# Optimization experiments

Hardware: AMD Instinct MI355X
Metric: run time of the kernel (lower is better)

Reference implementation:

```python
import jax, jax.numpy as jnp
import numpy as np

B, S, C, DM, NH, DH = 1, 2048, 2048, 768, 12, 64
LN_EPS = 1e-9


def setup_inputs() -> dict:
    rng = jax.random.key(0)
    ks = jax.random.split(rng, 24)
    f32 = jnp.float32
    p = 0.02  # param init scale
    inp = {
        'query': jax.random.normal(ks[0], (B, S, DM), f32),
        'key': jax.random.normal(ks[1], (B, C, DM), f32),
        'value': jax.random.normal(ks[2], (B, C, DM), f32),
        'phi': jax.random.normal(ks[3], (S, DM), f32) * p,
        'pi': jax.random.normal(ks[4], (S, DM), f32) * p,
        'psi': jax.random.normal(ks[5], (C, DM), f32) * p,
        'omega': jax.random.normal(ks[6], (C, DM), f32) * p,
        'cls_mask': jnp.ones((S, C), f32),
        'token_type_mat': jax.random.randint(ks[7], (B, S, C), 0, 2).astype(bool),
        'attention_mask': jnp.ones((B, C), jnp.int32),
        # learned parameters
        'Wq': jax.random.normal(ks[8], (DM, NH * DH), f32) * p,
        'Wk': jax.random.normal(ks[9], (DM, NH * DH), f32) * p,
        'bk': jnp.zeros((NH * DH,), f32),
        'Wv': jax.random.normal(ks[10], (DM, NH * DH), f32) * p,
        'bv': jnp.zeros((NH * DH,), f32),
        'r_w_bias': jax.random.normal(ks[11], (NH, DH), f32) * p,
        'r_r_bias': jax.random.normal(ks[12], (NH, DH), f32) * p,
        'r_kernel': jax.random.normal(ks[13], (DM, NH, DH), f32) * p,
        'r_s_bias': jax.random.normal(ks[14], (NH, DH), f32) * p,
        'seg_embed': jax.random.normal(ks[15], (2, NH, DH), f32) * p,
        'Wo': jax.random.normal(ks[16], (NH * DH, DM), f32) * p,
        'bo': jnp.zeros((DM,), f32),
        'ln_scale': jnp.ones((DM,), f32),
        'ln_bias': jnp.zeros((DM,), f32),
    }
    return inp


def reference(query, key, value, phi, pi, psi, omega, cls_mask,
              token_type_mat, attention_mask,
              Wq, Wk, bk, Wv, bv, r_w_bias, r_r_bias, r_kernel,
              r_s_bias, seg_embed, Wo, bo, ln_scale, ln_bias):
    b, s, _ = query.shape
    c = key.shape[1]
    scale = 1.0 / DH ** 0.5
    # head projections
    q = (query @ Wq).reshape(b, s, NH, DH) * scale          # [b,i,n,h]
    k = (key @ Wk + bk).reshape(b, c, NH, DH)                # [b,j,n,h]
    v = (value @ Wv + bv).reshape(b, c, NH, DH)
    # content score
    content = jnp.einsum('binh,bjnh->bnij', q + r_w_bias * scale, k)
    # factorized relative positional attention
    qr = jnp.einsum('binh,dnh->bind', q + r_r_bias * scale, r_kernel)  # [b,i,n,d_model]
    pos = (jnp.einsum('bind,jd->bnij', qr * phi[:, None], psi)
           + jnp.einsum('bind,jd->bnij', qr * pi[:, None], omega))
    pos = pos * cls_mask
    # token-type attention
    tt_bias = jnp.einsum('binh,snh->bnis', q + r_s_bias * scale, seg_embed)  # [b,n,i,2]
    diff_tt, same_tt = jnp.split(tt_bias, 2, axis=-1)  # each [b,n,i,1]
    tt = jnp.where(token_type_mat[:, None], same_tt, diff_tt) * cls_mask
    # combine, mask, softmax
    score = content + pos + tt
    score = score - 1000000.0 * (1.0 - attention_mask[:, None, None].astype(jnp.float32))
    prob = jax.nn.softmax(score, axis=-1)  # [b,n,i,j]
    attn_vec = jnp.einsum('bnij,bjnh->binh', prob, v).reshape(b, s, NH * DH)
    attn_out = attn_vec @ Wo + bo
    # residual + layernorm
    x = query + attn_out
    mu = x.mean(-1, keepdims=True)
    var = x.var(-1, keepdims=True)
    return (x - mu) * jax.lax.rsqrt(var + LN_EPS) * ln_scale + ln_bias
```

## Files before the change

kernel.cpp:

```cpp
#include <hip/hip_runtime.h>
#include <hip/hip_bf16.h>
#include <stddef.h>

#define DEVINL __device__ __forceinline__

typedef __attribute__((ext_vector_type(8))) short short8;
typedef __attribute__((ext_vector_type(4))) float f32x4;

static constexpr int S_LEN = 2048;
static constexpr int C_LEN = 2048;
static constexpr int DMODEL = 768;
static constexpr int NHEAD = 12;
static constexpr int DHEAD = 64;
static constexpr float SCALE = 0.125f;

DEVINL float bf2f(short s) {
    union { unsigned u; float f; } v;
    v.u = ((unsigned)(unsigned short)s) << 16;
    return v.f;
}
DEVINL short f2bf(float f) {
    union { float f; unsigned u; } v;
    v.f = f;
    unsigned r = v.u + 0x7FFFu + ((v.u >> 16) & 1u);
    return (short)(r >> 16);
}
DEVINL f32x4 zero4() { f32x4 z; z[0]=0.f; z[1]=0.f; z[2]=0.f; z[3]=0.f; return z; }

DEVINL int swz(int width, int row, int col) {
    return (row * width + col) ^ ((row & 7) << 3);
}

DEVINL void gl_lds16(const short* g, short* l) {
    __builtin_amdgcn_global_load_lds(
        (const __attribute__((address_space(1))) void*)g,
        (__attribute__((address_space(3))) void*)l,
        16, 0, 0);
}

template<int ROWS, int WIDTH>
DEVINL void stage_lds_swz(short* lds_tile, const short* src, int src_stride, int w, int lane) {
    constexpr int CPR = WIDTH / 8;
    constexpr int CH  = ROWS * CPR;
    for (int c0 = w * 64; c0 < CH; c0 += 256) {
        int chunk = c0 + lane;
        int row   = chunk / CPR;
        int ccol  = chunk % CPR;
        int scol  = ccol ^ (row & 7);
        gl_lds16(src + (size_t)row * src_stride + scol * 8, lds_tile + c0 * 8);
    }
}

DEVINL void stage_addcol(short* dst, const short* src, const float* p1, const float* p2,
                         int col0, int src_stride) {
    for (int c = threadIdx.x; c < 1024; c += 256) {
        int row = c >> 3;
        int cc  = (c & 7) * 8;
        short8 a = *(const short8*)(src + (size_t)row * src_stride + cc);
        short8 r;
#pragma unroll
        for (int e = 0; e < 8; ++e)
            r[e] = f2bf(bf2f(a[e]) + (p1[col0 + cc + e] - p2[col0 + cc + e]) * SCALE);
        *(short8*)(dst + swz(64, row, cc)) = r;
    }
}

DEVINL void mfma_step_128(const short* As, const short* Bs, f32x4 acc[4][4],
                          int wr, int wc, int lane) {
#pragma unroll
    for (int kk = 0; kk < 64; kk += 32) {
        short8 a[4], b[4];
#pragma unroll
        for (int mi = 0; mi < 4; ++mi)
            a[mi] = *(const short8*)(As + swz(64, wr*64 + mi*16 + (lane & 15), kk + (lane >> 4) * 8));
#pragma unroll
        for (int ni = 0; ni < 4; ++ni)
            b[ni] = *(const short8*)(Bs + swz(64, wc*64 + ni*16 + (lane & 15), kk + (lane >> 4) * 8));
#pragma unroll
        for (int mi = 0; mi < 4; ++mi)
#pragma unroll
            for (int ni = 0; ni < 4; ++ni)
                acc[mi][ni] = __builtin_amdgcn_mfma_f32_16x16x32_bf16(a[mi], b[ni], acc[mi][ni], 0, 0, 0);
    }
}

DEVINL void mfma_row16(const short* As, const short* Bs, f32x4 acc[8], int w, int lane) {
#pragma unroll
    for (int kk = 0; kk < 64; kk += 32) {
        short8 a = *(const short8*)(As + swz(64, w*16 + (lane & 15), kk + (lane >> 4) * 8));
#pragma unroll
        for (int nj = 0; nj < 8; ++nj) {
            short8 b = *(const short8*)(Bs + swz(64, nj*16 + (lane & 15), kk + (lane >> 4) * 8));
            acc[nj] = __builtin_amdgcn_mfma_f32_16x16x32_bf16(a, b, acc[nj], 0, 0, 0);
        }
    }
}

template<int KSTEPS>
DEVINL void gemm128_body(const short* A, const short* Bt, short* As, short* Bs,
                         f32x4 acc[4][4], int wr, int wc, int lane, int w) {
    for (int ks = 0; ks < KSTEPS; ++ks) {
        if (ks) __syncthreads();
        stage_lds_swz<128, 64>(As, A + ks * 64, DMODEL, w, lane);
        stage_lds_swz<128, 64>(Bs, Bt + ks * 64, DMODEL, w, lane);
        __syncthreads();
        mfma_step_128(As, Bs, acc, wr, wc, lane);
    }
}

__global__ void conv_kernel(const float* q, const float* k, const float* v,
                            const float* psi, const float* omega, const float* rk,
                            short* qc, short* kc, short* vc,
                            short* psc, short* omc, short* rkc) {
    int z = blockIdx.z;
    const float* src; short* dst; int n4;
    switch (z) {
        case 0: src = q;     dst = qc;  n4 = 393216; break;
        case 1: src = k;     dst = kc;  n4 = 393216; break;
        case 2: src = v;     dst = vc;  n4 = 393216; break;
        case 3: src = psi;   dst = psc; n4 = 393216; break;
        case 4: src = omega; dst = omc; n4 = 393216; break;
        default: src = rk;   dst = rkc; n4 = 147456; break;
    }
    for (int i = blockIdx.x * 256 + threadIdx.x; i < n4; i += gridDim.x * 256) {
        float4 f = *(const float4*)(src + (size_t)i * 4);
        short4 o;
        o.x = f2bf(f.x); o.y = f2bf(f.y); o.z = f2bf(f.z); o.w = f2bf(f.w);
        *(short4*)(dst + (size_t)i * 4) = o;
    }
}

__global__ void transpose_kernel(const float* wq, const float* wk, const float* wv, const float* wo,
                                 short* wqt, short* wkt, short* wvt, short* wot) {
    __shared__ float tile[64][65];
    int z = blockIdx.z;
    const float* src = (z == 0) ? wq : (z == 1) ? wk : (z == 2) ? wv : wo;
    short*       dst = (z == 0) ? wqt : (z == 1) ? wkt : (z == 2) ? wvt : wot;
    int r0 = blockIdx.x * 64, c0 = blockIdx.y * 64;
    for (int e = threadIdx.x; e < 4096; e += 256) {
        int rr = e >> 6, cc = e & 63;
        tile[rr][cc] = src[(size_t)(r0 + rr) * DMODEL + c0 + cc];
    }
    __syncthreads();
    for (int e = threadIdx.x; e < 4096; e += 256) {
        int rr = e >> 6, cc = e & 63;
        dst[(size_t)(c0 + rr) * DMODEL + r0 + cc] = f2bf(tile[cc][rr]);
    }
}

__global__ __launch_bounds__(256, 2)
void qkv_kernel(const short* qc, const short* kc, const short* vc,
                const short* wqt, const short* wkt, const short* wvt,
                const float* bk, const float* bv, const float* rw,
                short* qw_a, short* kpack, short* vt) {
    __shared__ short As[128 * 64], Bs[128 * 64];
    int z = blockIdx.z;
    const short* A  = (z == 0) ? qc  : (z == 1) ? kc  : vc;
    const short* Bt = (z == 0) ? wqt : (z == 1) ? wkt : wvt;
    int i0 = blockIdx.x * 128, c0 = blockIdx.y * 128;
    int t = threadIdx.x, lane = t & 63, w = t >> 6, wr = w >> 1, wc = w & 1;

    f32x4 acc[4][4];
#pragma unroll
    for (int mi = 0; mi < 4; ++mi)
#pragma unroll
        for (int ni = 0; ni < 4; ++ni) acc[mi][ni] = zero4();

    gemm128_body<12>(A + (size_t)i0 * DMODEL, Bt + (size_t)c0 * DMODEL, As, Bs, acc, wr, wc, lane, w);

#pragma unroll
    for (int mi = 0; mi < 4; ++mi)
#pragma unroll
        for (int ni = 0; ni < 4; ++ni)
#pragma unroll
            for (int r = 0; r < 4; ++r) {
                int row = i0 + wr*64 + mi*16 + ((lane >> 4) << 2) + r;
                int col = c0 + wc*64 + ni*16 + (lane & 15);
                float v = acc[mi][ni][r];
                if (z == 0) {
                    qw_a[(size_t)row * DMODEL + col] = f2bf(v * SCALE + rw[col] * SCALE);
                } else if (z == 1) {
                    float vv = v + bk[col];
                    kpack[((size_t)(col >> 6) * C_LEN + row) * DHEAD + (col & 63)] = f2bf(vv);
                } else {
                    float vv = v + bv[col];
                    vt[((size_t)(col >> 6) * DHEAD + (col & 63)) * C_LEN + row] = f2bf(vv);
                }
            }
}

__global__ __launch_bounds__(256, 2)
void qr_kernel(const short* qwa, const short* rkc, const float* rr, const float* rw,
               const float* phi, const float* pi_, short* a1, short* a2, int n_base) {
    __shared__ short As[128 * 64], Bs[128 * 64];
    int nl = blockIdx.z, n = n_base + nl;
    int i0 = blockIdx.x * 128, d0 = blockIdx.y * 128;
    int t = threadIdx.x, lane = t & 63, w = t >> 6, wr = w >> 1, wc = w & 1;

    f32x4 acc[4][4];
#pragma unroll
    for (int mi = 0; mi < 4; ++mi)
#pragma unroll
        for (int ni = 0; ni < 4; ++ni) acc[mi][ni] = zero4();

    stage_addcol(As, qwa + (size_t)i0 * DMODEL + n * DHEAD, rr, rw, n * DHEAD, DMODEL);
    stage_lds_swz<128, 64>(Bs, rkc + (size_t)d0 * DMODEL + n * DHEAD, DMODEL, w, lane);
    __syncthreads();
    mfma_step_128(As, Bs, acc, wr, wc, lane);

#pragma unroll
    for (int mi = 0; mi < 4; ++mi)
#pragma unroll
        for (int ni = 0; ni < 4; ++ni)
#pragma unroll
            for (int r = 0; r < 4; ++r) {
                int row = i0 + wr*64 + mi*16 + ((lane >> 4) << 2) + r;
                int col = d0 + wc*64 + ni*16 + (lane & 15);
                float v = acc[mi][ni][r];
                size_t src = (size_t)row * DMODEL + col;
                size_t dst = ((size_t)nl * S_LEN + row) * DMODEL + col;
                a1[dst] = f2bf(v * phi[src]);
                a2[dst] = f2bf(v * pi_[src]);
            }
}

__global__ void ttb_kernel(const short* qwa, const float* seg, const float* rs, const float* rw,
                           float* ttd, float* tts) {
    int idx = blockIdx.x * 256 + threadIdx.x;
    int n = idx >> 11, i = idx & 2047;
    const short* q  = qwa + (size_t)i * DMODEL + n * DHEAD;
    const float* e0 = seg + n * DHEAD;
    const float* e1 = seg + NHEAD * DHEAD + n * DHEAD;
    float s0 = 0.f, s1 = 0.f;
#pragma unroll
    for (int h = 0; h < DHEAD; ++h) {
        float qv = bf2f(q[h]) + (rs[n * DHEAD + h] - rw[n * DHEAD + h]) * SCALE;
        s0 += qv * e0[h];
        s1 += qv * e1[h];
    }
    ttd[n * S_LEN + i] = s0;
    tts[n * S_LEN + i] = s1;
}

__global__ __launch_bounds__(256, 2)
void flash_kernel(const short* qw_a, const short* kpack, const short* a1, const short* a2,
                  const short* psc, const short* omc, const float* cls_mask,
                  const int* ttmat, const int* amask, const float* ttd, const float* tts,
                  const short* vt, short* pacc, float* pm, float* pl, int n_base) {
    __shared__ short dbuf[2 * 12288];
    __shared__ short Ps[64 * 128];

    int orig = blockIdx.x;
    int sid  = (orig & 7) * 192 + (orig >> 3);
    int jt = sid & 15;
    int q6 = sid >> 4;
    int nl = q6 % 3;
    int i0 = (q6 / 3) * 64;
    int n  = n_base + nl;
    int j0 = jt * 128;

    int t = threadIdx.x, lane = t & 63, w = t >> 6;
    int lrow = lane >> 4;
    int lcol = lane & 15;

    f32x4 acc_c[8], acc_p[8];
#pragma unroll
    for (int nj = 0; nj < 8; ++nj) { acc_c[nj] = zero4(); acc_p[nj] = zero4(); }

    const short* a_base = a1 + ((size_t)nl * S_LEN + i0) * DMODEL;
    const short* a2base = a2 + ((size_t)nl * S_LEN + i0) * DMODEL;
    const short* p_base = psc + (size_t)j0 * DMODEL;
    const short* o_base = omc + (size_t)j0 * DMODEL;

    auto STAGE = [&](int b, int s) {
        short* B = dbuf + b * 12288;
        if (s == 0) {
            stage_lds_swz<64, 64>(B, qw_a + (size_t)i0 * DMODEL + n * DHEAD, DMODEL, w, lane);
            stage_lds_swz<128, 64>(B + 4096, kpack + ((size_t)n * C_LEN + j0) * DHEAD, DHEAD, w, lane);
        } else {
            int d0 = ((s - 1) % 12) * 64;
            const short* asrc = ((s <= 12) ? a_base : a2base) + d0;
            const short* bsrc = ((s <= 12) ? p_base : o_base) + d0;
            stage_lds_swz<64, 64>(B, asrc, DMODEL, w, lane);
            stage_lds_swz<128, 64>(B + 4096, bsrc, DMODEL, w, lane);
        }
    };

    STAGE(0, 0);
    STAGE(1, 1);

    for (int ks = 0; ks < 25; ++ks) {
        int cur = ks & 1;
        short* B = dbuf + cur * 12288;
        if (ks < 24) { asm volatile("s_waitcnt vmcnt(6)" ::: "memory"); }
        else         { asm volatile("s_waitcnt vmcnt(4)" ::: "memory"); }
        __builtin_amdgcn_sched_barrier(0);
        __builtin_amdgcn_s_barrier();
        if (ks == 0) mfma_row16(B, B + 4096, acc_c, w, lane);
        else         mfma_row16(B, B + 4096, acc_p, w, lane);
        asm volatile("s_waitcnt lgkmcnt(0)" ::: "memory");
        __builtin_amdgcn_sched_barrier(0);
        __builtin_amdgcn_s_barrier();
        if (ks < 23)
            STAGE(cur, ks + 2);
        else if (ks == 23)
            stage_lds_swz<64, 128>(dbuf + 12288, vt + (size_t)(n * DHEAD) * C_LEN + j0, C_LEN, w, lane);
    }

    int iBase = i0 + w*16 + lrow*4;
    float tdiff[4], tsame[4];
#pragma unroll
    for (int r = 0; r < 4; ++r) {
        tdiff[r] = ttd[n * S_LEN + iBase + r];
        tsame[r] = tts[n * S_LEN + iBase + r];
    }
    float pbuf[8][4];
    float m[4] = { -1.0e9f, -1.0e9f, -1.0e9f, -1.0e9f };
#pragma unroll
    for (int nj = 0; nj < 8; ++nj) {
        int jg = j0 + nj*16 + lcol;
        float pen = 1.0e6f * (1.0f - (float)amask[jg]);
#pragma unroll
        for (int r = 0; r < 4; ++r) {
            size_t eidx = (size_t)(iBase + r) * C_LEN + jg;
            float clsv = cls_mask[eidx];
            float ttv  = ttmat[eidx] ? tsame[r] : tdiff[r];
            float sc = acc_c[nj][r] + clsv * (acc_p[nj][r] + ttv) - pen;
            pbuf[nj][r] = sc;
            m[r] = fmaxf(m[r], sc);
        }
    }
#pragma unroll
    for (int r = 0; r < 4; ++r) {
        float v = m[r];
        v = fmaxf(v, __shfl_xor(v, 1));
        v = fmaxf(v, __shfl_xor(v, 2));
        v = fmaxf(v, __shfl_xor(v, 4));
        v = fmaxf(v, __shfl_xor(v, 8));
        m[r] = v;
    }
    float l[4] = { 0.f, 0.f, 0.f, 0.f };
#pragma unroll
    for (int nj = 0; nj < 8; ++nj)
#pragma unroll
        for (int r = 0; r < 4; ++r) {
            float pv = __expf(fminf(pbuf[nj][r] - m[r], 0.0f));
            pbuf[nj][r] = pv;
            l[r] += pv;
        }
#pragma unroll
    for (int r = 0; r < 4; ++r) {
        float v = l[r];
        v += __shfl_xor(v, 1);
        v += __shfl_xor(v, 2);
        v += __shfl_xor(v, 4);
        v += __shfl_xor(v, 8);
        l[r] = v;
    }

#pragma unroll
    for (int nj = 0; nj < 8; ++nj)
#pragma unroll
        for (int r = 0; r < 4; ++r)
            Ps[swz(128, w*16 + lrow*4 + r, nj*16 + lcol)] = f2bf(pbuf[nj][r]);

    __syncthreads();

    f32x4 out_acc[4];
#pragma unroll
    for (int x = 0; x < 4; ++x) out_acc[x] = zero4();
#pragma unroll
    for (int kk = 0; kk < 4; ++kk) {
        short8 pa = *(const short8*)(Ps + swz(128, w*16 + lcol, kk*32 + lrow*8));
#pragma unroll
        for (int nh = 0; nh < 4; ++nh) {
            short8 vb = *(const short8*)(dbuf + 12288 + swz(128, nh*16 + lcol, kk*32 + lrow*8));
            out_acc[nh] = __builtin_amdgcn_mfma_f32_16x16x32_bf16(pa, vb, out_acc[nh], 0, 0, 0);
        }
    }

#pragma unroll
    for (int r = 0; r < 4; ++r) {
        int ig = i0 + w*16 + lrow*4 + r;
        size_t base = ((size_t)(nl * S_LEN + ig) * 16 + jt);
        if (lcol == 0) { pm[base] = m[r]; pl[base] = l[r]; }
#pragma unroll
        for (int nh = 0; nh < 4; ++nh)
            pacc[base * 64 + nh*16 + lcol] = f2bf(out_acc[nh][r]);
    }
}

__global__ void combine_kernel(const short* pacc, const float* pm, const float* pl,
                               short* avec, int n_base) {
    int idx = blockIdx.x * 256 + threadIdx.x;
    int h8 = idx & 7;
    int rest = idx >> 3;
    int i  = rest & 2047;
    int nl = rest >> 11;
    size_t b = ((size_t)nl * S_LEN + i) * 16;
    float M = -1.0e30f;
#pragma unroll
    for (int p = 0; p < 16; ++p) M = fmaxf(M, pm[b + p]);
    float L = 0.f;
    float o[8] = {0.f,0.f,0.f,0.f,0.f,0.f,0.f,0.f};
#pragma unroll
    for (int p = 0; p < 16; ++p) {
        float wg = __expf(pm[b + p] - M);
        L += wg * pl[b + p];
        short8 v = *(const short8*)(pacc + (b + p) * 64 + h8 * 8);
#pragma unroll
        for (int e = 0; e < 8; ++e) o[e] += wg * bf2f(v[e]);
    }
    float invL = 1.0f / L;
    short8 r;
#pragma unroll
    for (int e = 0; e < 8; ++e) r[e] = f2bf(o[e] * invL);
    *(short8*)(avec + (size_t)i * DMODEL + (n_base + nl) * DHEAD + h8 * 8) = r;
}

__global__ __launch_bounds__(256, 2)
void outproj_kernel(const short* avec, const short* wot, const float* bo,
                    const float* query, float* X) {
    __shared__ short As[128 * 64], Bs[128 * 64];
    int i0 = blockIdx.x * 128, c0 = blockIdx.y * 128;
    int t = threadIdx.x, lane = t & 63, w = t >> 6, wr = w >> 1, wc = w & 1;

    f32x4 acc[4][4];
#pragma unroll
    for (int mi = 0; mi < 4; ++mi)
#pragma unroll
        for (int ni = 0; ni < 4; ++ni) acc[mi][ni] = zero4();

    gemm128_body<12>(avec + (size_t)i0 * DMODEL, wot + (size_t)c0 * DMODEL, As, Bs, acc, wr, wc, lane, w);

#pragma unroll
    for (int mi = 0; mi < 4; ++mi)
#pragma unroll
        for (int ni = 0; ni < 4; ++ni)
#pragma unroll
            for (int r = 0; r < 4; ++r) {
                int row = i0 + wr*64 + mi*16 + ((lane >> 4) << 2) + r;
                int col = c0 + wc*64 + ni*16 + (lane & 15);
                float v = acc[mi][ni][r] + bo[col];
                X[(size_t)row * DMODEL + col] = v + query[(size_t)row * DMODEL + col];
            }
}

__global__ void ln_kernel(const float* X, const float* gam, const float* bet, float* out) {
    int row = blockIdx.x, t = threadIdx.x;
    const float* xr = X + (size_t)row * DMODEL;
    float x0 = xr[t], x1 = xr[t + 256], x2 = xr[t + 512];
    float s = x0 + x1 + x2;
    float q = x0*x0 + x1*x1 + x2*x2;
#pragma unroll
    for (int d = 1; d < 64; d <<= 1) { s += __shfl_xor(s, d); q += __shfl_xor(q, d); }
    __shared__ float rs_[4], rq_[4];
    int w = t >> 6, lane = t & 63;
    if (lane == 0) { rs_[w] = s; rq_[w] = q; }
    __syncthreads();
    s = rs_[0] + rs_[1] + rs_[2] + rs_[3];
    q = rq_[0] + rq_[1] + rq_[2] + rq_[3];
    float mu  = s * (1.0f / 768.0f);
    float var = q * (1.0f / 768.0f) - mu * mu;
    float rstd = rsqrtf(fmaxf(var, 0.0f) + 1e-9f);
    out[(size_t)row * DMODEL + t]       = (x0 - mu) * rstd * gam[t]       + bet[t];
    out[(size_t)row * DMODEL + t + 256] = (x1 - mu) * rstd * gam[t + 256] + bet[t + 256];
    out[(size_t)row * DMODEL + t + 512] = (x2 - mu) * rstd * gam[t + 512] + bet[t + 512];
}

extern "C" void kernel_launch(void* const* d_in, const int* in_sizes, int n_in,
                              void* d_out, int out_size, void* d_ws, size_t ws_size,
                              hipStream_t stream) {
    const float* query = (const float*)d_in[0];
    const float* key   = (const float*)d_in[1];
    const float* value = (const float*)d_in[2];
    const float* phi   = (const float*)d_in[3];
    const float* pi_   = (const float*)d_in[4];
    const float* psi   = (const float*)d_in[5];
    const float* omega = (const float*)d_in[6];
    const float* cls   = (const float*)d_in[7];
    const int*   ttm   = (const int*)d_in[8];
    const int*   am    = (const int*)d_in[9];
    const float* Wq    = (const float*)d_in[10];
    const float* Wk    = (const float*)d_in[11];
    const float* bk    = (const float*)d_in[12];
    const float* Wv    = (const float*)d_in[13];
    const float* bv    = (const float*)d_in[14];
    const float* rw    = (const float*)d_in[15];
    const float* rr    = (const float*)d_in[16];
    const float* rk    = (const float*)d_in[17];
    const float* rs    = (const float*)d_in[18];
    const float* seg   = (const float*)d_in[19];
    const float* Wo    = (const float*)d_in[20];
    const float* bo    = (const float*)d_in[21];
    const float* lng   = (const float*)d_in[22];
    const float* lnb   = (const float*)d_in[23];

    char* ws = (char*)d_ws;
    constexpr size_t SZ_W   = 768ull * 768 * 2;
    constexpr size_t SZ_SD  = 2048ull * 768 * 2;
    constexpr size_t SZ_3H  = 3ull * 2048 * 768 * 2;
    constexpr size_t OFF_WQT = 0;
    constexpr size_t OFF_WKT = OFF_WQT + SZ_W;
    constexpr size_t OFF_WVT = OFF_WKT + SZ_W;
    constexpr size_t OFF_WOT = OFF_WVT + SZ_W;
    constexpr size_t OFF_RKC = OFF_WOT + SZ_W;
    constexpr size_t OFF_QC  = OFF_RKC + SZ_W;
    constexpr size_t OFF_KC  = OFF_QC  + SZ_SD;
    constexpr size_t OFF_VC  = OFF_KC  + SZ_SD;
    constexpr size_t OFF_PSC = OFF_VC  + SZ_SD;
    constexpr size_t OFF_OMC = OFF_PSC + SZ_SD;
    constexpr size_t OFF_QWA = OFF_OMC + SZ_SD;
    constexpr size_t OFF_KP  = OFF_QWA + SZ_SD;
    constexpr size_t OFF_VT  = OFF_KP  + SZ_SD;
    constexpr size_t OFF_A1  = OFF_VT  + SZ_SD;
    constexpr size_t OFF_A2  = OFF_A1  + SZ_3H;
    constexpr size_t OFF_TTD = OFF_A2  + SZ_3H;
    constexpr size_t OFF_TTS = OFF_TTD + 12ull * 2048 * 4;
    constexpr size_t OFF_AV  = OFF_TTS + 12ull * 2048 * 4;
    constexpr size_t OFF_PA  = OFF_AV  + SZ_SD;
    constexpr size_t OFF_PM  = OFF_PA  + 3ull * 2048 * 16 * 64 * 2;
    constexpr size_t OFF_PL  = OFF_PM  + 3ull * 2048 * 16 * 4;
    constexpr size_t OFF_X   = OFF_PA;
    constexpr size_t NEED    = OFF_PL + 3ull * 2048 * 16 * 4;

    if (ws_size < NEED) return;

    short* wqt  = (short*)(ws + OFF_WQT);
    short* wkt  = (short*)(ws + OFF_WKT);
    short* wvt  = (short*)(ws + OFF_WVT);
    short* wot  = (short*)(ws + OFF_WOT);
    short* rkc  = (short*)(ws + OFF_RKC);
    short* qc   = (short*)(ws + OFF_QC);
    short* kc   = (short*)(ws + OFF_KC);
    short* vc   = (short*)(ws + OFF_VC);
    short* psc  = (short*)(ws + OFF_PSC);
    short* omc  = (short*)(ws + OFF_OMC);
    short* qwa  = (short*)(ws + OFF_QWA);
    short* kp   = (short*)(ws + OFF_KP);
    short* vt   = (short*)(ws + OFF_VT);
    short* a1   = (short*)(ws + OFF_A1);
    short* a2   = (short*)(ws + OFF_A2);
    float* ttd  = (float*)(ws + OFF_TTD);
    float* tts  = (float*)(ws + OFF_TTS);
    short* avec = (short*)(ws + OFF_AV);
    short* pacc = (short*)(ws + OFF_PA);
    float* pm   = (float*)(ws + OFF_PM);
    float* pl   = (float*)(ws + OFF_PL);
    float* X    = (float*)(ws + OFF_X);

    conv_kernel<<<dim3(768, 1, 6), 256, 0, stream>>>(query, key, value, psi, omega, rk,
                                                     qc, kc, vc, psc, omc, rkc);
    transpose_kernel<<<dim3(12, 12, 4), 256, 0, stream>>>(Wq, Wk, Wv, Wo, wqt, wkt, wvt, wot);
    qkv_kernel<<<dim3(16, 6, 3), 256, 0, stream>>>(qc, kc, vc, wqt, wkt, wvt,
                                                   bk, bv, rw, qwa, kp, vt);
    ttb_kernel<<<96, 256, 0, stream>>>(qwa, seg, rs, rw, ttd, tts);
    for (int nb = 0; nb < NHEAD; nb += 3) {
        qr_kernel<<<dim3(16, 6, 3), 256, 0, stream>>>(qwa, rkc, rr, rw, phi, pi_, a1, a2, nb);
        flash_kernel<<<dim3(1536), 256, 0, stream>>>(qwa, kp, a1, a2, psc, omc, cls,
                                                     ttm, am, ttd, tts, vt, pacc, pm, pl, nb);
        combine_kernel<<<192, 256, 0, stream>>>(pacc, pm, pl, avec, nb);
    }
    outproj_kernel<<<dim3(16, 6), 256, 0, stream>>>(avec, wot, bo, query, X);
    ln_kernel<<<2048, 256, 0, stream>>>(X, lng, lnb, (float*)d_out);
}
```

Before: 546.3 us.

## Use 2x2 wave tiling in flash kernel and compress mask inputs

The flash kernel's per-wave tiling changes from 16 rows by 128 columns to a 2x2 layout of 32 rows by 64 columns. This cuts LDS fragment reads per MFMA, and each wave now emits its own partial softmax, so the combine step merges 32 partials instead of 16. The cls mask and token-type matrix are converted once to bf16 and int8 to shrink their repeated reads across the four head-group launches. The separate P buffer now aliases the staging buffer, freeing LDS so occupancy can rise to 3 blocks per CU, and the grid becomes 3D instead of the swizzled 1D order. In exchange it adds conversion work, larger partial buffers and more combine traffic, and the bf16 cls mask is lossy only for values that are not exactly representable.

```diff
diff --git a/kernel.cpp b/kernel.cpp
--- a/kernel.cpp
+++ b/kernel.cpp
@@ -84,15 +84,22 @@
     }
 }
 
-DEVINL void mfma_row16(const short* As, const short* Bs, f32x4 acc[8], int w, int lane) {
+DEVINL void mfma_2x2(const short* As, const short* Bs, f32x4 acc[2][4],
+                     int wr2, int wc2, int lane) {
 #pragma unroll
     for (int kk = 0; kk < 64; kk += 32) {
-        short8 a = *(const short8*)(As + swz(64, w*16 + (lane & 15), kk + (lane >> 4) * 8));
-#pragma unroll
-        for (int nj = 0; nj < 8; ++nj) {
-            short8 b = *(const short8*)(Bs + swz(64, nj*16 + (lane & 15), kk + (lane >> 4) * 8));
-            acc[nj] = __builtin_amdgcn_mfma_f32_16x16x32_bf16(a, b, acc[nj], 0, 0, 0);
-        }
+        short8 a[2], b[4];
+#pragma unroll
+        for (int mi = 0; mi < 2; ++mi)
+            a[mi] = *(const short8*)(As + swz(64, wr2*32 + mi*16 + (lane & 15), kk + (lane >> 4) * 8));
+#pragma unroll
+        for (int nj = 0; nj < 4; ++nj)
+            b[nj] = *(const short8*)(Bs + swz(64, wc2*64 + nj*16 + (lane & 15), kk + (lane >> 4) * 8));
+#pragma unroll
+        for (int mi = 0; mi < 2; ++mi)
+#pragma unroll
+            for (int nj = 0; nj < 4; ++nj)
+                acc[mi][nj] = __builtin_amdgcn_mfma_f32_16x16x32_bf16(a[mi], b[nj], acc[mi][nj], 0, 0, 0);
     }
 }
 
@@ -110,17 +117,29 @@
 
 __global__ void conv_kernel(const float* q, const float* k, const float* v,
                             const float* psi, const float* omega, const float* rk,
+                            const float* cls, const int* ttm,
                             short* qc, short* kc, short* vc,
-                            short* psc, short* omc, short* rkc) {
+                            short* psc, short* omc, short* rkc,
+                            short* clsb, char* ttm8) {
     int z = blockIdx.z;
+    if (z == 7) {
+        for (int i = blockIdx.x * 256 + threadIdx.x; i < 1048576; i += gridDim.x * 256) {
+            int4 t = *(const int4*)(ttm + (size_t)i * 4);
+            char4 o;
+            o.x = (char)t.x; o.y = (char)t.y; o.z = (char)t.z; o.w = (char)t.w;
+            *(char4*)(ttm8 + (size_t)i * 4) = o;
+        }
+        return;
+    }
     const float* src; short* dst; int n4;
     switch (z) {
-        case 0: src = q;     dst = qc;  n4 = 393216; break;
-        case 1: src = k;     dst = kc;  n4 = 393216; break;
-        case 2: src = v;     dst = vc;  n4 = 393216; break;
-        case 3: src = psi;   dst = psc; n4 = 393216; break;
-        case 4: src = omega; dst = omc; n4 = 393216; break;
-        default: src = rk;   dst = rkc; n4 = 147456; break;
+        case 0: src = q;     dst = qc;   n4 = 393216;  break;
+        case 1: src = k;     dst = kc;   n4 = 393216;  break;
+        case 2: src = v;     dst = vc;   n4 = 393216;  break;
+        case 3: src = psi;   dst = psc;  n4 = 393216;  break;
+        case 4: src = omega; dst = omc;  n4 = 393216;  break;
+        case 5: src = rk;    dst = rkc;  n4 = 147456;  break;
+        default: src = cls;  dst = clsb; n4 = 1048576; break;
     }
     for (int i = blockIdx.x * 256 + threadIdx.x; i < n4; i += gridDim.x * 256) {
         float4 f = *(const float4*)(src + (size_t)i * 4);
@@ -242,30 +261,29 @@
     tts[n * S_LEN + i] = s1;
 }
 
-__global__ __launch_bounds__(256, 2)
+__global__ __launch_bounds__(256, 3)
 void flash_kernel(const short* qw_a, const short* kpack, const short* a1, const short* a2,
-                  const short* psc, const short* omc, const float* cls_mask,
-                  const int* ttmat, const int* amask, const float* ttd, const float* tts,
+                  const short* psc, const short* omc, const short* clsb,
+                  const char* ttm8, const int* amask, const float* ttd, const float* tts,
                   const short* vt, short* pacc, float* pm, float* pl, int n_base) {
     __shared__ short dbuf[2 * 12288];
-    __shared__ short Ps[64 * 128];
-
-    int orig = blockIdx.x;
-    int sid  = (orig & 7) * 192 + (orig >> 3);
-    int jt = sid & 15;
-    int q6 = sid >> 4;
-    int nl = q6 % 3;
-    int i0 = (q6 / 3) * 64;
-    int n  = n_base + nl;
+    short* Ps = dbuf;
+
+    int nl = blockIdx.y, n = n_base + nl;
+    int i0 = blockIdx.x * 64;
+    int jt = blockIdx.z;
     int j0 = jt * 128;
 
     int t = threadIdx.x, lane = t & 63, w = t >> 6;
+    int wr2 = w >> 1, wc2 = w & 1;
     int lrow = lane >> 4;
     int lcol = lane & 15;
 
-    f32x4 acc_c[8], acc_p[8];
-#pragma unroll
-    for (int nj = 0; nj < 8; ++nj) { acc_c[nj] = zero4(); acc_p[nj] = zero4(); }
+    f32x4 acc_c[2][4], acc_p[2][4];
+#pragma unroll
+    for (int mi = 0; mi < 2; ++mi)
+#pragma unroll
+        for (int nj = 0; nj < 4; ++nj) { acc_c[mi][nj] = zero4(); acc_p[mi][nj] = zero4(); }
 
     const short* a_base = a1 + ((size_t)nl * S_LEN + i0) * DMODEL;
     const short* a2base = a2 + ((size_t)nl * S_LEN + i0) * DMODEL;
@@ -296,8 +314,8 @@
         else         { asm volatile("s_waitcnt vmcnt(4)" ::: "memory"); }
         __builtin_amdgcn_sched_barrier(0);
         __builtin_amdgcn_s_barrier();
-        if (ks == 0) mfma_row16(B, B + 4096, acc_c, w, lane);
-        else         mfma_row16(B, B + 4096, acc_p, w, lane);
+        if (ks == 0) mfma_2x2(B, B + 4096, acc_c, wr2, wc2, lane);
+        else         mfma_2x2(B, B + 4096, acc_p, wr2, wc2, lane);
         asm volatile("s_waitcnt lgkmcnt(0)" ::: "memory");
         __builtin_amdgcn_sched_barrier(0);
         __builtin_amdgcn_s_barrier();
@@ -307,87 +325,118 @@
             stage_lds_swz<64, 128>(dbuf + 12288, vt + (size_t)(n * DHEAD) * C_LEN + j0, C_LEN, w, lane);
     }
 
-    int iBase = i0 + w*16 + lrow*4;
-    float tdiff[4], tsame[4];
-#pragma unroll
-    for (int r = 0; r < 4; ++r) {
-        tdiff[r] = ttd[n * S_LEN + iBase + r];
-        tsame[r] = tts[n * S_LEN + iBase + r];
-    }
-    float pbuf[8][4];
-    float m[4] = { -1.0e9f, -1.0e9f, -1.0e9f, -1.0e9f };
-#pragma unroll
-    for (int nj = 0; nj < 8; ++nj) {
-        int jg = j0 + nj*16 + lcol;
+    float tdiff[2][4], tsame[2][4];
+#pragma unroll
+    for (int mi = 0; mi < 2; ++mi)
+#pragma unroll
+        for (int r = 0; r < 4; ++r) {
+            int ig = i0 + wr2*32 + mi*16 + lrow*4 + r;
+            tdiff[mi][r] = ttd[n * S_LEN + ig];
+            tsame[mi][r] = tts[n * S_LEN + ig];
+        }
+    float pbuf[2][4][4];
+    float m[2][4];
+#pragma unroll
+    for (int mi = 0; mi < 2; ++mi)
+#pragma unroll
+        for (int r = 0; r < 4; ++r) m[mi][r] = -1.0e9f;
+#pragma unroll
+    for (int nj = 0; nj < 4; ++nj) {
+        int jg = j0 + wc2*64 + nj*16 + lcol;
         float pen = 1.0e6f * (1.0f - (float)amask[jg]);
 #pragma unroll
+        for (int mi = 0; mi < 2; ++mi)
+#pragma unroll
+            for (int r = 0; r < 4; ++r) {
+                int ig = i0 + wr2*32 + mi*16 + lrow*4 + r;
+                size_t eidx = (size_t)ig * C_LEN + jg;
+                float clsv = bf2f(clsb[eidx]);
+                float ttv  = ttm8[eidx] ? tsame[mi][r] : tdiff[mi][r];
+                float sc = acc_c[mi][nj][r] + clsv * (acc_p[mi][nj][r] + ttv) - pen;
+                pbuf[mi][nj][r] = sc;
+                m[mi][r] = fmaxf(m[mi][r], sc);
+            }
+    }
+#pragma unroll
+    for (int mi = 0; mi < 2; ++mi)
+#pragma unroll
         for (int r = 0; r < 4; ++r) {
-            size_t eidx = (size_t)(iBase + r) * C_LEN + jg;
-            float clsv = cls_mask[eidx];
-            float ttv  = ttmat[eidx] ? tsame[r] : tdiff[r];
-            float sc = acc_c[nj][r] + clsv * (acc_p[nj][r] + ttv) - pen;
-            pbuf[nj][r] = sc;
-            m[r] = fmaxf(m[r], sc);
+            float v = m[mi][r];
+            v = fmaxf(v, __shfl_xor(v, 1));
+            v = fmaxf(v, __shfl_xor(v, 2));
+            v = fmaxf(v, __shfl_xor(v, 4));
+            v = fmaxf(v, __shfl_xor(v, 8));
+            m[mi][r] = v;
         }
-    }
-#pragma unroll
-    for (int r = 0; r < 4; ++r) {
-        float v = m[r];
-        v = fmaxf(v, __shfl_xor(v, 1));
-        v = fmaxf(v, __shfl_xor(v, 2));
-        v = fmaxf(v, __shfl_xor(v, 4));
-        v = fmaxf(v, __shfl_xor(v, 8));
-        m[r] = v;
-    }
-    float l[4] = { 0.f, 0.f, 0.f, 0.f };
-#pragma unroll
-    for (int nj = 0; nj < 8; ++nj)
+    float l[2][4];
+#pragma unroll
+    for (int mi = 0; mi < 2; ++mi)
+#pragma unroll
+        for (int r = 0; r < 4; ++r) l[mi][r] = 0.f;
+#pragma unroll
+    for (int nj = 0; nj < 4; ++nj)
+#pragma unroll
+        for (int mi = 0; mi < 2; ++mi)
+#pragma unroll
+            for (int r = 0; r < 4; ++r) {
+                float pv = __expf(fminf(pbuf[mi][nj][r] - m[mi][r], 0.0f));
+                pbuf[mi][nj][r] = pv;
+                l[mi][r] += pv;
+            }
+#pragma unroll
+    for (int mi = 0; mi < 2; ++mi)
 #pragma unroll
         for (int r = 0; r < 4; ++r) {
-            float pv = __expf(fminf(pbuf[nj][r] - m[r], 0.0f));
-            pbuf[nj][r] = pv;
-            l[r] += pv;
+            float v = l[mi][r];
+            v += __shfl_xor(v, 1);
+            v += __shfl_xor(v, 2);
+            v += __shfl_xor(v, 4);
+            v += __shfl_xor(v, 8);
+            l[mi][r] = v;
         }
-#pragma unroll
-    for (int r = 0; r < 4; ++r) {
-        float v = l[r];
-        v += __shfl_xor(v, 1);
-        v += __shfl_xor(v, 2);
-        v += __shfl_xor(v, 4);
-        v += __shfl_xor(v, 8);
-        l[r] = v;
-    }
-
-#pragma unroll
-    for (int nj = 0; nj < 8; ++nj)
-#pragma unroll
-        for (int r = 0; r < 4; ++r)
-            Ps[swz(128, w*16 + lrow*4 + r, nj*16 + lcol)] = f2bf(pbuf[nj][r]);
+
+#pragma unroll
+    for (int mi = 0; mi < 2; ++mi)
+#pragma unroll
+        for (int nj = 0; nj < 4; ++nj)
+#pragma unroll
+            for (int r = 0; r < 4; ++r)
+                Ps[swz(128, wr2*32 + mi*16 + lrow*4 + r, wc2*64 + nj*16 + lcol)] = f2bf(pbuf[mi][nj][r]);
 
     __syncthreads();
 
-    f32x4 out_acc[4];
-#pragma unroll
-    for (int x = 0; x < 4; ++x) out_acc[x] = zero4();
-#pragma unroll
-    for (int kk = 0; kk < 4; ++kk) {
-        short8 pa = *(const short8*)(Ps + swz(128, w*16 + lcol, kk*32 + lrow*8));
+    f32x4 out_acc[2][4];
+#pragma unroll
+    for (int mi = 0; mi < 2; ++mi)
+#pragma unroll
+        for (int nh = 0; nh < 4; ++nh) out_acc[mi][nh] = zero4();
+#pragma unroll
+    for (int kk = 0; kk < 2; ++kk) {
+        short8 pa[2];
+#pragma unroll
+        for (int mi = 0; mi < 2; ++mi)
+            pa[mi] = *(const short8*)(Ps + swz(128, wr2*32 + mi*16 + (lane & 15), wc2*64 + kk*32 + lrow*8));
 #pragma unroll
         for (int nh = 0; nh < 4; ++nh) {
-            short8 vb = *(const short8*)(dbuf + 12288 + swz(128, nh*16 + lcol, kk*32 + lrow*8));
-            out_acc[nh] = __builtin_amdgcn_mfma_f32_16x16x32_bf16(pa, vb, out_acc[nh], 0, 0, 0);
+            short8 vb = *(const short8*)(dbuf + 12288 + swz(128, nh*16 + (lane & 15), wc2*64 + kk*32 + lrow*8));
+#pragma unroll
+            for (int mi = 0; mi < 2; ++mi)
+                out_acc[mi][nh] = __builtin_amdgcn_mfma_f32_16x16x32_bf16(pa[mi], vb, out_acc[mi][nh], 0, 0, 0);
         }
     }
 
-#pragma unroll
-    for (int r = 0; r < 4; ++r) {
-        int ig = i0 + w*16 + lrow*4 + r;
-        size_t base = ((size_t)(nl * S_LEN + ig) * 16 + jt);
-        if (lcol == 0) { pm[base] = m[r]; pl[base] = l[r]; }
-#pragma unroll
-        for (int nh = 0; nh < 4; ++nh)
-            pacc[base * 64 + nh*16 + lcol] = f2bf(out_acc[nh][r]);
-    }
+    int jp = jt * 2 + wc2;
+#pragma unroll
+    for (int mi = 0; mi < 2; ++mi)
+#pragma unroll
+        for (int r = 0; r < 4; ++r) {
+            int ig = i0 + wr2*32 + mi*16 + lrow*4 + r;
+            size_t base = ((size_t)(nl * S_LEN + ig) * 32 + jp);
+            if (lcol == 0) { pm[base] = m[mi][r]; pl[base] = l[mi][r]; }
+#pragma unroll
+            for (int nh = 0; nh < 4; ++nh)
+                pacc[base * 64 + nh*16 + lcol] = f2bf(out_acc[mi][nh][r]);
+        }
 }
 
 __global__ void combine_kernel(const short* pacc, const float* pm, const float* pl,
@@ -397,14 +446,14 @@
     int rest = idx >> 3;
     int i  = rest & 2047;
     int nl = rest >> 11;
-    size_t b = ((size_t)nl * S_LEN + i) * 16;
+    size_t b = ((size_t)nl * S_LEN + i) * 32;
     float M = -1.0e30f;
 #pragma unroll
-    for (int p = 0; p < 16; ++p) M = fmaxf(M, pm[b + p]);
+    for (int p = 0; p < 32; ++p) M = fmaxf(M, pm[b + p]);
     float L = 0.f;
     float o[8] = {0.f,0.f,0.f,0.f,0.f,0.f,0.f,0.f};
 #pragma unroll
-    for (int p = 0; p < 16; ++p) {
+    for (int p = 0; p < 32; ++p) {
         float wg = __expf(pm[b + p] - M);
         L += wg * pl[b + p];
         short8 v = *(const short8*)(pacc + (b + p) * 64 + h8 * 8);
@@ -515,14 +564,16 @@
     constexpr size_t OFF_VT  = OFF_KP  + SZ_SD;
     constexpr size_t OFF_A1  = OFF_VT  + SZ_SD;
     constexpr size_t OFF_A2  = OFF_A1  + SZ_3H;
-    constexpr size_t OFF_TTD = OFF_A2  + SZ_3H;
+    constexpr size_t OFF_CLB = OFF_A2  + SZ_3H;
+    constexpr size_t OFF_TT8 = OFF_CLB + 2048ull * 2048 * 2;
+    constexpr size_t OFF_TTD = OFF_TT8 + 2048ull * 2048;
     constexpr size_t OFF_TTS = OFF_TTD + 12ull * 2048 * 4;
     constexpr size_t OFF_AV  = OFF_TTS + 12ull * 2048 * 4;
     constexpr size_t OFF_PA  = OFF_AV  + SZ_SD;
-    constexpr size_t OFF_PM  = OFF_PA  + 3ull * 2048 * 16 * 64 * 2;
-    constexpr size_t OFF_PL  = OFF_PM  + 3ull * 2048 * 16 * 4;
+    constexpr size_t OFF_PM  = OFF_PA  + 3ull * 2048 * 32 * 64 * 2;
+    constexpr size_t OFF_PL  = OFF_PM  + 3ull * 2048 * 32 * 4;
     constexpr size_t OFF_X   = OFF_PA;
-    constexpr size_t NEED    = OFF_PL + 3ull * 2048 * 16 * 4;
+    constexpr size_t NEED    = OFF_PL + 3ull * 2048 * 32 * 4;
 
     if (ws_size < NEED) return;
 
@@ -541,6 +592,8 @@
     short* vt   = (short*)(ws + OFF_VT);
     short* a1   = (short*)(ws + OFF_A1);
     short* a2   = (short*)(ws + OFF_A2);
+    short* clsb = (short*)(ws + OFF_CLB);
+    char*  ttm8 = (char*)(ws + OFF_TT8);
     float* ttd  = (float*)(ws + OFF_TTD);
     float* tts  = (float*)(ws + OFF_TTS);
     short* avec = (short*)(ws + OFF_AV);
@@ -549,16 +602,16 @@
     float* pl   = (float*)(ws + OFF_PL);
     float* X    = (float*)(ws + OFF_X);
 
-    conv_kernel<<<dim3(768, 1, 6), 256, 0, stream>>>(query, key, value, psi, omega, rk,
-                                                     qc, kc, vc, psc, omc, rkc);
+    conv_kernel<<<dim3(768, 1, 8), 256, 0, stream>>>(query, key, value, psi, omega, rk, cls, ttm,
+                                                     qc, kc, vc, psc, omc, rkc, clsb, ttm8);
     transpose_kernel<<<dim3(12, 12, 4), 256, 0, stream>>>(Wq, Wk, Wv, Wo, wqt, wkt, wvt, wot);
     qkv_kernel<<<dim3(16, 6, 3), 256, 0, stream>>>(qc, kc, vc, wqt, wkt, wvt,
                                                    bk, bv, rw, qwa, kp, vt);
     ttb_kernel<<<96, 256, 0, stream>>>(qwa, seg, rs, rw, ttd, tts);
     for (int nb = 0; nb < NHEAD; nb += 3) {
         qr_kernel<<<dim3(16, 6, 3), 256, 0, stream>>>(qwa, rkc, rr, rw, phi, pi_, a1, a2, nb);
-        flash_kernel<<<dim3(1536), 256, 0, stream>>>(qwa, kp, a1, a2, psc, omc, cls,
-                                                     ttm, am, ttd, tts, vt, pacc, pm, pl, nb);
+        flash_kernel<<<dim3(32, 3, 16), 256, 0, stream>>>(qwa, kp, a1, a2, psc, omc, clsb,
+                                                          ttm8, am, ttd, tts, vt, pacc, pm, pl, nb);
         combine_kernel<<<192, 256, 0, stream>>>(pacc, pm, pl, avec, nb);
     }
     outproj_kernel<<<dim3(16, 6), 256, 0, stream>>>(avec, wot, bo, query, X);
```

Measured after the change: 461.3 us. -15.6%, faster.
